# Kernel tuning notes

Measured on AMD Instinct MI355X. Metric: run time of the kernel, lower is better.

The kernel has to match this reference:

```python
import jax, jax.numpy as jnp
import numpy as np

N, IN_C, HEADS, OUT_C = 100000, 128, 4, 64
E = 1600000
NEG_SLOPE = 0.2
BN_EPS = 1e-5


def setup_inputs() -> dict:
    key = jax.random.key(0)
    ks = jax.random.split(key, 8)
    x = jax.random.normal(ks[0], (N, IN_C), dtype=jnp.float32)
    edge_index = jax.random.randint(ks[1], (2, E), 0, N, dtype=jnp.int64)
    glorot = 1.0 / np.sqrt(IN_C)
    W = jax.random.uniform(ks[2], (IN_C, HEADS * OUT_C), dtype=jnp.float32, minval=-glorot, maxval=glorot)
    att_src = jax.random.normal(ks[3], (HEADS, OUT_C), dtype=jnp.float32) * 0.1
    att_dst = jax.random.normal(ks[4], (HEADS, OUT_C), dtype=jnp.float32) * 0.1
    bias = jnp.zeros((HEADS * OUT_C,), dtype=jnp.float32)
    gamma = jnp.ones((HEADS * OUT_C,), dtype=jnp.float32)
    beta = jnp.zeros((HEADS * OUT_C,), dtype=jnp.float32)
    return {"x": x, "edge_index": edge_index, "W": W, "att_src": att_src,
            "att_dst": att_dst, "bias": bias, "gamma": gamma, "beta": beta}


def reference(x, edge_index, W, att_src, att_dst, bias, gamma, beta):
    n = x.shape[0]
    h_dim, c_dim = att_src.shape
    # add self loops
    loops = jnp.arange(n, dtype=edge_index.dtype)
    src = jnp.concatenate([edge_index[0], loops])  # [Et]
    dst = jnp.concatenate([edge_index[1], loops])  # [Et]
    # linear projection per head
    h = (x @ W).reshape(n, h_dim, c_dim)  # [N,H,C]
    a_src = jnp.einsum('nhc,hc->nh', h, att_src)  # [N,H]
    a_dst = jnp.einsum('nhc,hc->nh', h, att_dst)  # [N,H]
    # edge-wise attention logits + LeakyReLU
    e = jax.nn.leaky_relu(a_src[src] + a_dst[dst], NEG_SLOPE)  # [Et,H]
    # segment softmax over destination neighborhoods
    m = jax.ops.segment_max(e, dst, num_segments=n)  # [N,H]
    e = jnp.exp(e - m[dst])
    denom = jax.ops.segment_sum(e, dst, num_segments=n)  # [N,H]
    alpha = e / (denom[dst] + 1e-16)  # [Et,H]
    # weighted scatter-add aggregation
    out = jax.ops.segment_sum(h[src] * alpha[:, :, None], dst, num_segments=n)  # [N,H,C]
    out = out.reshape(n, h_dim * c_dim) + bias
    # BatchNorm (training-mode batch statistics) + ELU
    mean = out.mean(axis=0)
    var = out.var(axis=0)
    out = gamma * (out - mean) * jax.lax.rsqrt(var + BN_EPS) + beta
    return jax.nn.elu(out)
```

## Files before the change

kernel.cpp:

```cpp
#include <hip/hip_runtime.h>

#define IN_C 128
#define HEADS 4
#define OUT_C 64
#define OUT_F 256
#define NEG_SLOPE 0.2f
#define BN_EPS 1e-5f
#define NBUCK 64
#define BSTRIDE 48

typedef __attribute__((ext_vector_type(8))) short short8;
typedef __attribute__((ext_vector_type(4))) float floatx4;

__device__ __forceinline__ unsigned short f2bf(float f) {
    unsigned u = __float_as_uint(f);
    u += 0x7FFF + ((u >> 16) & 1);
    return (unsigned short)(u >> 16);
}
__device__ __forceinline__ float bf2f(unsigned short u) {
    return __uint_as_float(((unsigned)u) << 16);
}

__global__ void wtprep_kernel(const float* __restrict__ W, unsigned short* __restrict__ Wp)
{
    int idx = blockIdx.x * blockDim.x + threadIdx.x;
    int j  = idx & 7;
    int l  = (idx >> 3) & 63;
    int nt = (idx >> 9) & 3;
    int kt = (idx >> 11) & 3;
    int w  = idx >> 13;
    int k   = kt * 32 + (l >> 4) * 8 + j;
    int col = w * 64 + nt * 16 + (l & 15);
    Wp[idx] = f2bf(W[(size_t)k * OUT_F + col]);
}

__global__ __launch_bounds__(256) void gemm_build_kernel(
    const float* __restrict__ x, const unsigned short* __restrict__ Wp,
    const float* __restrict__ att_src, const float* __restrict__ att_dst,
    unsigned short* __restrict__ h, float* __restrict__ a_src, float* __restrict__ a_dst,
    const int* __restrict__ ei, int* __restrict__ deg, int* __restrict__ srcs,
    int nbg, int n, int E)
{
    if ((int)blockIdx.x >= nbg) {
        int t8 = (((int)blockIdx.x - nbg) * 256 + (int)threadIdx.x) * 8;
        if (t8 < E) {
            int4 s0 = *(const int4*)(ei + t8);
            int4 s1 = *(const int4*)(ei + t8 + 4);
            int4 d0 = *(const int4*)(ei + E + t8);
            int4 d1 = *(const int4*)(ei + E + t8 + 4);
            int ss[8] = {s0.x, s0.y, s0.z, s0.w, s1.x, s1.y, s1.z, s1.w};
            int dd[8] = {d0.x, d0.y, d0.z, d0.w, d1.x, d1.y, d1.z, d1.w};
#pragma unroll
            for (int u = 0; u < 8; ++u) {
                int pos = atomicAdd(&deg[dd[u]], 1);
                if (pos < BSTRIDE) srcs[dd[u] * BSTRIDE + pos] = ss[u];
            }
        }
        return;
    }

    __shared__ unsigned short As[16][144];
    __shared__ unsigned short Hs[16][268];

    const int t = threadIdx.x;
    const int w = t >> 6;
    const int l = t & 63;
    const int quad = l >> 4;
    const int c15 = l & 15;
    const int base = blockIdx.x * 64;

    float4 xv[8];
    {
        const size_t maxf4 = (size_t)n * 32 - 1;
#pragma unroll
        for (int i = 0; i < 8; ++i) {
            size_t f4 = (size_t)base * 32 + (size_t)(t + i * 256);
            xv[i] = ((const float4*)x)[(f4 <= maxf4) ? f4 : maxf4];
        }
    }

    short8 bfrag[4][4];
#pragma unroll
    for (int kt = 0; kt < 4; ++kt)
#pragma unroll
        for (int nt = 0; nt < 4; ++nt)
            bfrag[kt][nt] = *(const short8*)(Wp + (((w * 4 + kt) * 4 + nt) << 9) + l * 8);

#pragma unroll
    for (int s = 0; s < 4; ++s) {
        const int tbase = base + s * 16;
        if (tbase >= n) break;

#pragma unroll
        for (int i = 0; i < 2; ++i) {
            int idx = t + i * 256;
            float4 v = xv[s * 2 + i];
            int fi = idx * 4;
            int row = fi >> 7, k = fi & 127;
            ushort4 b;
            b.x = f2bf(v.x); b.y = f2bf(v.y); b.z = f2bf(v.z); b.w = f2bf(v.w);
            *(ushort4*)&As[row][k] = b;
        }
        __syncthreads();

        floatx4 acc[4] = {};
#pragma unroll
        for (int kt = 0; kt < 4; ++kt) {
            int k0 = kt * 32 + quad * 8;
            short8 afrag = *(const short8*)&As[c15][k0];
#pragma unroll
            for (int nt = 0; nt < 4; ++nt)
                acc[nt] = __builtin_amdgcn_mfma_f32_16x16x32_bf16(afrag, bfrag[kt][nt], acc[nt], 0, 0, 0);
        }

        float asum[4] = {0.f, 0.f, 0.f, 0.f}, adsum[4] = {0.f, 0.f, 0.f, 0.f};
#pragma unroll
        for (int nt = 0; nt < 4; ++nt) {
            int col = w * 64 + nt * 16 + c15;
            float aw = att_src[col];
            float dw = att_dst[col];
#pragma unroll
            for (int r = 0; r < 4; ++r) {
                float v = acc[nt][r];
                Hs[quad * 4 + r][col] = f2bf(v);
                asum[r] = fmaf(v, aw, asum[r]);
                adsum[r] = fmaf(v, dw, adsum[r]);
            }
        }
#pragma unroll
        for (int r = 0; r < 4; ++r) {
            float vs = asum[r], vd = adsum[r];
#pragma unroll
            for (int m = 1; m < 16; m <<= 1) {
                vs += __shfl_xor(vs, m, 64);
                vd += __shfl_xor(vd, m, 64);
            }
            if (c15 == 0) {
                int node = tbase + quad * 4 + r;
                a_src[(size_t)node * HEADS + w] = vs;
                a_dst[(size_t)node * HEADS + w] = vd;
            }
        }
        __syncthreads();

#pragma unroll
        for (int i = 0; i < 2; ++i) {
            int chunk = t + i * 256;
            int si = chunk * 8;
            int row = si >> 8, c0 = si & 255;
            int4 v = *(const int4*)&Hs[row][c0];
            *(int4*)(h + (size_t)(tbase + row) * OUT_F + c0) = v;
        }
    }
}

__global__ __launch_bounds__(256) void agg_kernel(
    const unsigned short* __restrict__ h, const float* __restrict__ a_src,
    const float* __restrict__ a_dst, const int* __restrict__ deg,
    const int* __restrict__ srcs, const float* __restrict__ bias,
    float* __restrict__ out, float* __restrict__ sbuck, int n)
{
    __shared__ float red[2][4][OUT_F];

    int wave_in_blk = threadIdx.x >> 6;
    int lane = threadIdx.x & 63;
    int dst = blockIdx.x * 4 + wave_in_blk;
    int myh = lane >> 4;
    bool valid = (dst < n);

    float4 o4 = {0.f, 0.f, 0.f, 0.f};

    if (valid) {
        float adh = a_dst[(size_t)dst * HEADS + myh];

        float es = a_src[(size_t)dst * HEADS + myh] + adh;
        es = (es > 0.f) ? es : NEG_SLOPE * es;
        float wgt = __expf(es);
        ushort4 hv = ((const ushort4*)(h + (size_t)dst * OUT_F))[lane];
        float4 acc;
        acc.x = bf2f(hv.x) * wgt; acc.y = bf2f(hv.y) * wgt;
        acc.z = bf2f(hv.z) * wgt; acc.w = bf2f(hv.w) * wgt;
        float wsum = wgt;

        const int start = dst * BSTRIDE;
        int cnt = deg[dst];
        cnt = (cnt > BSTRIDE) ? BSTRIDE : cnt;
        const int last = start + cnt - 1;
        for (int j = 0; j < cnt; j += 8) {
            int rem = cnt - j;
            int s[8];
#pragma unroll
            for (int u = 0; u < 8; ++u) {
                int idx = start + j + u;
                s[u] = srcs[(idx < last) ? idx : last];
            }
            float ew[8];
#pragma unroll
            for (int u = 0; u < 8; ++u) ew[u] = a_src[(size_t)s[u] * HEADS + myh];
            ushort4 hh[8];
#pragma unroll
            for (int u = 0; u < 8; ++u) hh[u] = ((const ushort4*)(h + (size_t)s[u] * OUT_F))[lane];
#pragma unroll
            for (int u = 0; u < 8; ++u) {
                float e = ew[u] + adh;
                e = (e > 0.f) ? e : NEG_SLOPE * e;
                float wv = __expf(e);
                wv = (u < rem) ? wv : 0.f;
                acc.x = fmaf(bf2f(hh[u].x), wv, acc.x);
                acc.y = fmaf(bf2f(hh[u].y), wv, acc.y);
                acc.z = fmaf(bf2f(hh[u].z), wv, acc.z);
                acc.w = fmaf(bf2f(hh[u].w), wv, acc.w);
                wsum += wv;
            }
        }

        float inv = 1.f / (wsum + 1e-16f);
        float4 b4 = ((const float4*)bias)[lane];
        o4.x = fmaf(acc.x, inv, b4.x);
        o4.y = fmaf(acc.y, inv, b4.y);
        o4.z = fmaf(acc.z, inv, b4.z);
        o4.w = fmaf(acc.w, inv, b4.w);
        ((float4*)(out + (size_t)dst * OUT_F))[lane] = o4;
    }

    int c0 = lane * 4;
    *(float4*)&red[0][wave_in_blk][c0] = o4;
    float4 q4;
    q4.x = o4.x * o4.x; q4.y = o4.y * o4.y; q4.z = o4.z * o4.z; q4.w = o4.w * o4.w;
    *(float4*)&red[1][wave_in_blk][c0] = q4;
    __syncthreads();

    int t = threadIdx.x;
    float s  = red[0][0][t] + red[0][1][t] + red[0][2][t] + red[0][3][t];
    float s2 = red[1][0][t] + red[1][1][t] + red[1][2][t] + red[1][3][t];
    float* bk = sbuck + (size_t)(blockIdx.x & (NBUCK - 1)) * (2 * OUT_F);
    atomicAdd(&bk[t], s);
    atomicAdd(&bk[OUT_F + t], s2);
}

__global__ void statsfinal_kernel(const float* __restrict__ sbuck,
                                  const float* __restrict__ gamma,
                                  const float* __restrict__ beta,
                                  float* __restrict__ ss, int n)
{
    int c = threadIdx.x;
    float s = 0.f, s2 = 0.f;
    for (int b = 0; b < NBUCK; ++b) {
        s  += sbuck[(size_t)b * (2 * OUT_F) + c];
        s2 += sbuck[(size_t)b * (2 * OUT_F) + OUT_F + c];
    }
    float invn = 1.f / (float)n;
    float mean = s * invn;
    float var = s2 * invn - mean * mean;
    float sc = gamma[c] * rsqrtf(var + BN_EPS);
    ss[c] = sc;
    ss[OUT_F + c] = beta[c] - mean * sc;
}

__device__ __forceinline__ float elu1(float v) {
    return (v > 0.f) ? v : expm1f(v);
}

__global__ __launch_bounds__(256) void bn_elu_kernel(float* __restrict__ out,
                                                     const float* __restrict__ ss,
                                                     long long n4)
{
    long long idx = (long long)blockIdx.x * blockDim.x + threadIdx.x;
    if (idx >= n4) return;
    int col4 = (int)(idx & 63);
    float4 v = ((float4*)out)[idx];
    float4 sc = ((const float4*)ss)[col4];
    float4 sh = ((const float4*)(ss + OUT_F))[col4];
    v.x = elu1(fmaf(v.x, sc.x, sh.x));
    v.y = elu1(fmaf(v.y, sc.y, sh.y));
    v.z = elu1(fmaf(v.z, sc.z, sh.z));
    v.w = elu1(fmaf(v.w, sc.w, sh.w));
    ((float4*)out)[idx] = v;
}

extern "C" void kernel_launch(void* const* d_in, const int* in_sizes, int n_in,
                              void* d_out, int out_size, void* d_ws, size_t ws_size,
                              hipStream_t stream)
{
    const float* x       = (const float*)d_in[0];
    const int*   ei      = (const int*)d_in[1];
    const float* W       = (const float*)d_in[2];
    const float* att_src = (const float*)d_in[3];
    const float* att_dst = (const float*)d_in[4];
    const float* bias    = (const float*)d_in[5];
    const float* gamma   = (const float*)d_in[6];
    const float* beta    = (const float*)d_in[7];
    float* out = (float*)d_out;

    const int n = in_sizes[0] / IN_C;
    const int E = in_sizes[1] / 2;

    float* ws = (float*)d_ws;
    size_t o = 0;
    unsigned short* h  = (unsigned short*)(ws + o); o += (size_t)n * OUT_F / 2;
    unsigned short* Wp = (unsigned short*)(ws + o); o += IN_C * OUT_F / 2;
    float* a_src  = ws + o; o += (size_t)n * HEADS;
    float* a_dst  = ws + o; o += (size_t)n * HEADS;
    float* ss     = ws + o; o += 2 * OUT_F;
    int* srcs     = (int*)(ws + o); o += (size_t)n * BSTRIDE;
    int* deg      = (int*)(ws + o); o += n;
    float* sbuck  = ws + o; o += (size_t)NBUCK * 2 * OUT_F;

    hipMemsetAsync(deg, 0, ((size_t)n + (size_t)NBUCK * 2 * OUT_F) * sizeof(int), stream);

    const int nbg = (n + 63) / 64;
    const int nbe = (E + 2047) / 2048;

    wtprep_kernel<<<(IN_C * OUT_F) / 256, 256, 0, stream>>>(W, Wp);
    gemm_build_kernel<<<nbg + nbe, 256, 0, stream>>>(x, Wp, att_src, att_dst,
                                                     h, a_src, a_dst,
                                                     ei, deg, srcs, nbg, n, E);
    agg_kernel<<<(n + 3) / 4, 256, 0, stream>>>(h, a_src, a_dst, deg, srcs, bias, out, sbuck, n);
    statsfinal_kernel<<<1, 256, 0, stream>>>(sbuck, gamma, beta, ss, n);
    bn_elu_kernel<<<(int)(((long long)n * 64 + 255) / 256), 256, 0, stream>>>(out, ss, (long long)n * 64);
}
```

Baseline: 457.8 us.

## Fold attention vectors into projected weights and compute logits via extra MFMA

Precomputes W·att_src and W·att_dst as an extra bf16 B-fragment so wave 0 computes the per-node attention logits with one additional MFMA per k-tile, replacing the per-element FMAs and cross-lane shuffle reductions. The edge-bucketing blocks are moved ahead of the GEMM blocks in the grid and each thread now handles 16 edges instead of 8. Logits now come from bf16-rounded folded weights rather than from the bf16-rounded h, which slightly changes numerics.

After: 422.4 us. 7.7% less time.

```diff
diff --git a/kernel.cpp b/kernel.cpp
--- a/kernel.cpp
+++ b/kernel.cpp
@@ -21,39 +21,60 @@
     return __uint_as_float(((unsigned)u) << 16);
 }
 
-__global__ void wtprep_kernel(const float* __restrict__ W, unsigned short* __restrict__ Wp)
+__global__ void prep_kernel(const float* __restrict__ W,
+                            const float* __restrict__ att_src, const float* __restrict__ att_dst,
+                            unsigned short* __restrict__ Wp, unsigned short* __restrict__ WaP)
 {
     int idx = blockIdx.x * blockDim.x + threadIdx.x;
-    int j  = idx & 7;
-    int l  = (idx >> 3) & 63;
-    int nt = (idx >> 9) & 3;
-    int kt = (idx >> 11) & 3;
-    int w  = idx >> 13;
-    int k   = kt * 32 + (l >> 4) * 8 + j;
-    int col = w * 64 + nt * 16 + (l & 15);
-    Wp[idx] = f2bf(W[(size_t)k * OUT_F + col]);
+    if (idx < 32768) {
+        int j  = idx & 7;
+        int l  = (idx >> 3) & 63;
+        int nt = (idx >> 9) & 3;
+        int kt = (idx >> 11) & 3;
+        int w  = idx >> 13;
+        int k   = kt * 32 + (l >> 4) * 8 + j;
+        int col = w * 64 + nt * 16 + (l & 15);
+        Wp[idx] = f2bf(W[(size_t)k * OUT_F + col]);
+    } else if (idx < 32768 + 2048) {
+        int i  = idx - 32768;
+        int j  = i & 7;
+        int l  = (i >> 3) & 63;
+        int kt = i >> 9;
+        int k   = kt * 32 + (l >> 4) * 8 + j;
+        int col = l & 15;
+        float s = 0.f;
+        if (col < 8) {
+            int head = col & 3;
+            const float* att = (col < 4) ? att_src : att_dst;
+            const float* wrow = W + (size_t)k * OUT_F + head * 64;
+            const float* arow = att + head * 64;
+#pragma unroll 8
+            for (int c = 0; c < 64; ++c) s = fmaf(wrow[c], arow[c], s);
+        }
+        WaP[i] = f2bf(s);
+    }
 }
 
 __global__ __launch_bounds__(256) void gemm_build_kernel(
     const float* __restrict__ x, const unsigned short* __restrict__ Wp,
-    const float* __restrict__ att_src, const float* __restrict__ att_dst,
+    const unsigned short* __restrict__ WaP,
     unsigned short* __restrict__ h, float* __restrict__ a_src, float* __restrict__ a_dst,
     const int* __restrict__ ei, int* __restrict__ deg, int* __restrict__ srcs,
-    int nbg, int n, int E)
-{
-    if ((int)blockIdx.x >= nbg) {
-        int t8 = (((int)blockIdx.x - nbg) * 256 + (int)threadIdx.x) * 8;
-        if (t8 < E) {
-            int4 s0 = *(const int4*)(ei + t8);
-            int4 s1 = *(const int4*)(ei + t8 + 4);
-            int4 d0 = *(const int4*)(ei + E + t8);
-            int4 d1 = *(const int4*)(ei + E + t8 + 4);
-            int ss[8] = {s0.x, s0.y, s0.z, s0.w, s1.x, s1.y, s1.z, s1.w};
-            int dd[8] = {d0.x, d0.y, d0.z, d0.w, d1.x, d1.y, d1.z, d1.w};
-#pragma unroll
-            for (int u = 0; u < 8; ++u) {
-                int pos = atomicAdd(&deg[dd[u]], 1);
-                if (pos < BSTRIDE) srcs[dd[u] * BSTRIDE + pos] = ss[u];
+    int nbe, int n, int E)
+{
+    if ((int)blockIdx.x < nbe) {
+        int t16 = ((int)blockIdx.x * 256 + (int)threadIdx.x) * 16;
+        if (t16 < E) {
+            int sv[16], dv[16];
+#pragma unroll
+            for (int q = 0; q < 4; ++q) {
+                *(int4*)&sv[q * 4] = *(const int4*)(ei + t16 + q * 4);
+                *(int4*)&dv[q * 4] = *(const int4*)(ei + E + t16 + q * 4);
+            }
+#pragma unroll
+            for (int u = 0; u < 16; ++u) {
+                int pos = atomicAdd(&deg[dv[u]], 1);
+                if (pos < BSTRIDE) srcs[dv[u] * BSTRIDE + pos] = sv[u];
             }
         }
         return;
@@ -67,7 +88,7 @@
     const int l = t & 63;
     const int quad = l >> 4;
     const int c15 = l & 15;
-    const int base = blockIdx.x * 64;
+    const int base = ((int)blockIdx.x - nbe) * 64;
 
     float4 xv[8];
     {
@@ -85,6 +106,13 @@
 #pragma unroll
         for (int nt = 0; nt < 4; ++nt)
             bfrag[kt][nt] = *(const short8*)(Wp + (((w * 4 + kt) * 4 + nt) << 9) + l * 8);
+
+    short8 bfragA[4];
+    if (w == 0) {
+#pragma unroll
+        for (int kt = 0; kt < 4; ++kt)
+            bfragA[kt] = *(const short8*)(WaP + (kt << 9) + l * 8);
+    }
 
 #pragma unroll
     for (int s = 0; s < 4; ++s) {
@@ -104,6 +132,7 @@
         __syncthreads();
 
         floatx4 acc[4] = {};
+        floatx4 acca = {};
 #pragma unroll
         for (int kt = 0; kt < 4; ++kt) {
             int k0 = kt * 32 + quad * 8;
@@ -111,34 +140,25 @@
 #pragma unroll
             for (int nt = 0; nt < 4; ++nt)
                 acc[nt] = __builtin_amdgcn_mfma_f32_16x16x32_bf16(afrag, bfrag[kt][nt], acc[nt], 0, 0, 0);
-        }
-
-        float asum[4] = {0.f, 0.f, 0.f, 0.f}, adsum[4] = {0.f, 0.f, 0.f, 0.f};
+            if (w == 0)
+                acca = __builtin_amdgcn_mfma_f32_16x16x32_bf16(afrag, bfragA[kt], acca, 0, 0, 0);
+        }
+
 #pragma unroll
         for (int nt = 0; nt < 4; ++nt) {
             int col = w * 64 + nt * 16 + c15;
-            float aw = att_src[col];
-            float dw = att_dst[col];
+#pragma unroll
+            for (int r = 0; r < 4; ++r)
+                Hs[quad * 4 + r][col] = f2bf(acc[nt][r]);
+        }
+
+        if (w == 0 && c15 < 8) {
+            int hsel = c15 & 3;
+            float* ap = (c15 < 4) ? a_src : a_dst;
 #pragma unroll
             for (int r = 0; r < 4; ++r) {
-                float v = acc[nt][r];
-                Hs[quad * 4 + r][col] = f2bf(v);
-                asum[r] = fmaf(v, aw, asum[r]);
-                adsum[r] = fmaf(v, dw, adsum[r]);
-            }
-        }
-#pragma unroll
-        for (int r = 0; r < 4; ++r) {
-            float vs = asum[r], vd = adsum[r];
-#pragma unroll
-            for (int m = 1; m < 16; m <<= 1) {
-                vs += __shfl_xor(vs, m, 64);
-                vd += __shfl_xor(vd, m, 64);
-            }
-            if (c15 == 0) {
                 int node = tbase + quad * 4 + r;
-                a_src[(size_t)node * HEADS + w] = vs;
-                a_dst[(size_t)node * HEADS + w] = vd;
+                ap[((size_t)node << 2) + hsel] = acca[r];
             }
         }
         __syncthreads();
@@ -297,8 +317,9 @@
 
     float* ws = (float*)d_ws;
     size_t o = 0;
-    unsigned short* h  = (unsigned short*)(ws + o); o += (size_t)n * OUT_F / 2;
-    unsigned short* Wp = (unsigned short*)(ws + o); o += IN_C * OUT_F / 2;
+    unsigned short* h   = (unsigned short*)(ws + o); o += (size_t)n * OUT_F / 2;
+    unsigned short* Wp  = (unsigned short*)(ws + o); o += IN_C * OUT_F / 2;
+    unsigned short* WaP = (unsigned short*)(ws + o); o += 2048 / 2;
     float* a_src  = ws + o; o += (size_t)n * HEADS;
     float* a_dst  = ws + o; o += (size_t)n * HEADS;
     float* ss     = ws + o; o += 2 * OUT_F;
@@ -309,12 +330,12 @@
     hipMemsetAsync(deg, 0, ((size_t)n + (size_t)NBUCK * 2 * OUT_F) * sizeof(int), stream);
 
     const int nbg = (n + 63) / 64;
-    const int nbe = (E + 2047) / 2048;
-
-    wtprep_kernel<<<(IN_C * OUT_F) / 256, 256, 0, stream>>>(W, Wp);
-    gemm_build_kernel<<<nbg + nbe, 256, 0, stream>>>(x, Wp, att_src, att_dst,
+    const int nbe = (E / 16 + 255) / 256;
+
+    prep_kernel<<<(32768 + 2048) / 256, 256, 0, stream>>>(W, att_src, att_dst, Wp, WaP);
+    gemm_build_kernel<<<nbe + nbg, 256, 0, stream>>>(x, Wp, WaP,
                                                      h, a_src, a_dst,
-                                                     ei, deg, srcs, nbg, n, E);
+                                                     ei, deg, srcs, nbe, n, E);
     agg_kernel<<<(n + 3) / 4, 256, 0, stream>>>(h, a_src, a_dst, deg, srcs, bias, out, sbuck, n);
     statsfinal_kernel<<<1, 256, 0, stream>>>(sbuck, gamma, beta, ss, n);
     bn_elu_kernel<<<(int)(((long long)n * 64 + 255) / 256), 256, 0, stream>>>(out, ss, (long long)n * 64);
```
